# Kernel tuning notes

Hardware: AMD Instinct MI355X
Metric: run time of the kernel (lower is better)

## Reference

```python
import jax, jax.numpy as jnp
import numpy as np

E = 16   # num_experts
K = 4    # num_activated_experts
B, S, H, I = 4, 1024, 1024, 2048


def setup_inputs() -> dict:
    key = jax.random.key(0)
    k0, k1, k2, k3 = jax.random.split(key, 4)
    scale = 0.02
    return {
        "hidden_states": jax.random.normal(k0, (B, S, H), jnp.float32),
        "router_w": jax.random.normal(k1, (H, E), jnp.float32) * scale,
        "router_b": jnp.zeros((E,), jnp.float32),
        "w1": jax.random.normal(k2, (E, H, I), jnp.float32) * scale,
        "b1": jnp.zeros((E, I), jnp.float32),
        "w2": jax.random.normal(k3, (E, I, H), jnp.float32) * scale,
        "b2": jnp.zeros((E, H), jnp.float32),
    }


def reference(hidden_states, router_w, router_b, w1, b1, w2, b2):
    b, s, h = hidden_states.shape
    # router: softmax over experts, pick top-k, renormalize top-k weights
    logits = hidden_states @ router_w + router_b            # [B,S,E]
    probs = jax.nn.softmax(logits, axis=-1)
    topw, topi = jax.lax.top_k(probs, K)                    # [B,S,K]
    topw = topw / jnp.sum(topw, axis=-1, keepdims=True)
    # scatter top-k weights into dense per-expert combine weights [B,S,E]
    combine = jnp.sum(
        jax.nn.one_hot(topi, E, dtype=hidden_states.dtype) * topw[..., None],
        axis=2,
    )
    x = hidden_states.reshape(b * s, h)                     # [T,H]
    c = combine.reshape(b * s, E)                           # [T,E]

    def body(acc, expert):
        w1e, b1e, w2e, b2e, ce = expert
        hmid = jax.nn.gelu(x @ w1e + b1e, approximate=False)  # [T,I]
        return acc + (hmid @ w2e + b2e) * ce[:, None], None

    out, _ = jax.lax.scan(body, jnp.zeros_like(x), (w1, b1, w2, b2, c.T))
    return out.reshape(b, s, h)
```

## Files before the change

kernel.cpp:

```cpp
#include <hip/hip_runtime.h>

#define T_TOK 4096
#define H_DIM 1024
#define I_DIM 2048
#define E_NUM 16
#define K_TOP 4
#define BM 128
#define BK 32
#define MAX_TILES 144
#define PAD_PAIRS (MAX_TILES * BM)
#define RW_Q 4104

typedef __attribute__((ext_vector_type(8))) short s16x8;
typedef __attribute__((ext_vector_type(4))) float f32x4;
typedef __attribute__((ext_vector_type(4))) unsigned short u16x4;
typedef __attribute__((ext_vector_type(8))) unsigned short u16x8;

__device__ __forceinline__ unsigned short f2bf(float f) {
  unsigned u = __float_as_uint(f);
  u += 0x7fffu + ((u >> 16) & 1u);
  return (unsigned short)(u >> 16);
}

__device__ __forceinline__ void mfma_bf16(const s16x8& a, const s16x8& b, f32x4& c) {
  asm("v_mfma_f32_16x16x32_bf16 %0, %1, %2, %0" : "+v"(c) : "v"(a), "v"(b));
}

__device__ __forceinline__ void gld16(const void* g, void* l) {
  __builtin_amdgcn_global_load_lds(
      (const __attribute__((address_space(1))) unsigned int*)g,
      (__attribute__((address_space(3))) unsigned int*)l, 16, 0, 0);
}

__device__ __forceinline__ int tile_map(const int* counts, int ty, int* tsp) {
  int e = -1, acc = 0, base = 0;
#pragma unroll
  for (int ee = 0; ee < E_NUM; ++ee) {
    int tc = (counts[ee] + 127) >> 7;
    if (ty >= acc && ty < acc + tc) {
      e = ee;
      *tsp = base + ((ty - acc) << 7);
    }
    acc += tc;
    base += tc << 7;
  }
  return e;
}

__global__ __launch_bounds__(256) void cvt_kernel(const float* __restrict__ x,
                                                  unsigned short* __restrict__ xb) {
  size_t i = ((size_t)blockIdx.x * 256 + threadIdx.x) * 8;
  f32x4 a = *(const f32x4*)(x + i);
  f32x4 b = *(const f32x4*)(x + i + 4);
  u16x8 o;
  o[0] = f2bf(a[0]); o[1] = f2bf(a[1]); o[2] = f2bf(a[2]); o[3] = f2bf(a[3]);
  o[4] = f2bf(b[0]); o[5] = f2bf(b[1]); o[6] = f2bf(b[2]); o[7] = f2bf(b[3]);
  *(u16x8*)(xb + i) = o;
}

__global__ __launch_bounds__(256) void router_kernel(
    const float* __restrict__ x, const float* __restrict__ rw,
    const float* __restrict__ rb, int* __restrict__ topi,
    float* __restrict__ topw, int* __restrict__ counts) {
  __shared__ float rws[4 * RW_Q];
  const int tid = threadIdx.x;
  for (int idx = tid * 4; idx < H_DIM * E_NUM; idx += 256 * 4) {
    f32x4 v = *(const f32x4*)(rw + idx);
    int h = idx >> 4, e0 = idx & 15;
    *(f32x4*)&rws[(h >> 8) * RW_Q + (h & 255) * 16 + e0] = v;
  }
  __syncthreads();
  const int w = tid >> 6, l = tid & 63;
  const int e = l & 15, q = l >> 4;
  const float rbe = rb[e];
  const float* ldsb = &rws[q * RW_Q + e];
#pragma unroll
  for (int i = 0; i < 4; ++i) {
    const int t = blockIdx.x * 16 + w * 4 + i;
    const float* xr = x + (size_t)t * H_DIM + (q << 8);
    float acc = 0.f;
#pragma unroll 8
    for (int hh = 0; hh < 256; hh += 4) {
      f32x4 xv = *(const f32x4*)(xr + hh);
      acc += xv[0] * ldsb[(hh + 0) * 16];
      acc += xv[1] * ldsb[(hh + 1) * 16];
      acc += xv[2] * ldsb[(hh + 2) * 16];
      acc += xv[3] * ldsb[(hh + 3) * 16];
    }
    acc += __shfl_xor(acc, 16);
    acc += __shfl_xor(acc, 32);
    float logit = acc + rbe;
    float m = logit;
    m = fmaxf(m, __shfl_xor(m, 1));
    m = fmaxf(m, __shfl_xor(m, 2));
    m = fmaxf(m, __shfl_xor(m, 4));
    m = fmaxf(m, __shfl_xor(m, 8));
    float ex = expf(logit - m);
    int rank = 0;
    const int b16 = l & 48;
#pragma unroll
    for (int j = 0; j < 16; ++j) {
      float vj = __shfl(ex, b16 + j);
      rank += (vj > ex) || (vj == ex && j < e);
    }
    float sel = (rank < K_TOP) ? ex : 0.f;
    float subs = sel;
    subs += __shfl_xor(subs, 1);
    subs += __shfl_xor(subs, 2);
    subs += __shfl_xor(subs, 4);
    subs += __shfl_xor(subs, 8);
    if (q == 0 && rank < K_TOP) {
      topi[t * K_TOP + rank] = e;
      topw[t * K_TOP + rank] = ex / subs;
      atomicAdd(&counts[e], 1);
    }
  }
}

__global__ __launch_bounds__(256) void scatter_kernel(
    const int* __restrict__ topi, const float* __restrict__ topw,
    const int* __restrict__ counts, int* __restrict__ cursor,
    int* __restrict__ pairTok, float* __restrict__ pairW,
    int* __restrict__ pairPos) {
  int padBase[E_NUM];
  int base = 0;
#pragma unroll
  for (int ee = 0; ee < E_NUM; ++ee) {
    padBase[ee] = base;
    base += ((counts[ee] + 127) >> 7) << 7;
  }
  int t = blockIdx.x * 256 + threadIdx.x;
  if (t >= T_TOK) return;
#pragma unroll
  for (int k = 0; k < K_TOP; ++k) {
    int e = topi[t * K_TOP + k];
    int pos = atomicAdd(&cursor[e], 1);
    int idx = padBase[e] + pos;
    pairTok[idx] = t;
    pairW[idx] = topw[t * K_TOP + k];
    pairPos[t * K_TOP + k] = idx;
  }
}

__global__ __launch_bounds__(256) void transpose_kernel(
    const float* __restrict__ src, unsigned short* __restrict__ dst, int R,
    int C) {
  size_t es = (size_t)R * C;
  src += es * blockIdx.z;
  dst += es * blockIdx.z;
  int r0 = blockIdx.y * 64, c0 = blockIdx.x * 64;
  __shared__ float tle[64][65];
  int rr = threadIdx.x >> 4, cc = (threadIdx.x & 15) * 4;
#pragma unroll
  for (int i = 0; i < 4; ++i) {
    f32x4 v = *(const f32x4*)(src + (size_t)(r0 + rr + 16 * i) * C + c0 + cc);
    tle[rr + 16 * i][cc + 0] = v[0];
    tle[rr + 16 * i][cc + 1] = v[1];
    tle[rr + 16 * i][cc + 2] = v[2];
    tle[rr + 16 * i][cc + 3] = v[3];
  }
  __syncthreads();
#pragma unroll
  for (int i = 0; i < 4; ++i) {
    int oc = c0 + rr + 16 * i;
    u16x4 o;
    o[0] = f2bf(tle[cc + 0][rr + 16 * i]);
    o[1] = f2bf(tle[cc + 1][rr + 16 * i]);
    o[2] = f2bf(tle[cc + 2][rr + 16 * i]);
    o[3] = f2bf(tle[cc + 3][rr + 16 * i]);
    *(u16x4*)(dst + (size_t)oc * R + r0 + cc) = o;
  }
}

__global__ __launch_bounds__(256, 4) void gemm1_kernel(
    const unsigned short* __restrict__ xb, const unsigned short* __restrict__ w1t,
    const float* __restrict__ b1, unsigned short* __restrict__ hmid,
    const int* __restrict__ pairTok, const int* __restrict__ counts) {
  const int bid = blockIdx.x;
  const int lin = (bid & 7) * 288 + (bid >> 3);
  const int tx = lin & 15, ty = lin >> 4;
  int tsp = 0;
  const int e = tile_map(counts, ty, &tsp);
  if (e < 0) return;
  const int n0 = tx * 128;
  __shared__ unsigned short As[2][BM * BK];
  __shared__ unsigned short Bs[2][BM * BK];
  const int tid = threadIdx.x, w = tid >> 6, l = tid & 63;
  const int rbase = w * 16 + (l >> 2);
  const int segp = (l & 3) ^ ((l >> 3) & 3);
  int tok0 = pairTok[tsp + rbase];
  if (tok0 < 0) tok0 = 0;
  int tok1 = pairTok[tsp + rbase + 64];
  if (tok1 < 0) tok1 = 0;
  const char* gA0 = (const char*)(xb + (size_t)tok0 * H_DIM) + segp * 16;
  const char* gA1 = (const char*)(xb + (size_t)tok1 * H_DIM) + segp * 16;
  const unsigned short* wbase = w1t + (size_t)e * I_DIM * H_DIM;
  const char* gB0 = (const char*)(wbase + (size_t)(n0 + rbase) * H_DIM) + segp * 16;
  const char* gB1 = (const char*)(wbase + (size_t)(n0 + rbase + 64) * H_DIM) + segp * 16;

  f32x4 acc[4][4];
#pragma unroll
  for (int m = 0; m < 4; ++m)
#pragma unroll
    for (int n = 0; n < 4; ++n) acc[m][n] = f32x4{0.f, 0.f, 0.f, 0.f};

  const int wr = w >> 1, wc = w & 1, lrow = l & 15, g = l >> 4;
  const int gs = g ^ ((l >> 1) & 3);
  const int NK = H_DIM / BK;

  gld16(gA0, &As[0][w * 512]);
  gld16(gA1, &As[0][2048 + w * 512]);
  gld16(gB0, &Bs[0][w * 512]);
  gld16(gB1, &Bs[0][2048 + w * 512]);

  for (int kt = 0; kt < NK; ++kt) {
    __syncthreads();
    if (kt + 1 < NK) {
      const int kb = (kt + 1) * 64;
      const int nb = (kt + 1) & 1;
      gld16(gA0 + kb, &As[nb][w * 512]);
      gld16(gA1 + kb, &As[nb][2048 + w * 512]);
      gld16(gB0 + kb, &Bs[nb][w * 512]);
      gld16(gB1 + kb, &Bs[nb][2048 + w * 512]);
    }
    const int cb = kt & 1;
    const s16x8* Ap = (const s16x8*)As[cb];
    const s16x8* Bp = (const s16x8*)Bs[cb];
    s16x8 av[4], bv[4];
#pragma unroll
    for (int m = 0; m < 4; ++m) av[m] = Ap[(wr * 64 + m * 16 + lrow) * 4 + gs];
#pragma unroll
    for (int n = 0; n < 4; ++n) bv[n] = Bp[(wc * 64 + n * 16 + lrow) * 4 + gs];
#pragma unroll
    for (int m = 0; m < 4; ++m)
#pragma unroll
      for (int n = 0; n < 4; ++n) mfma_bf16(av[m], bv[n], acc[m][n]);
  }

  const float* b1e = b1 + (size_t)e * I_DIM;
#pragma unroll
  for (int m = 0; m < 4; ++m) {
    const int rw0 = wr * 64 + m * 16 + g * 4;
#pragma unroll
    for (int n = 0; n < 4; ++n) {
      const int col = n0 + wc * 64 + n * 16 + lrow;
      const float bb = b1e[col];
      f32x4 v = acc[m][n];
#pragma unroll
      for (int j = 0; j < 4; ++j) {
        const int p = tsp + rw0 + j;
        float xv = v[j] + bb;
        float y = 0.7978845608028654f * (xv + 0.044715f * xv * xv * xv);
        float ey = __expf(2.f * y);
        float th = 1.f - 2.f / (ey + 1.f);
        float ge = 0.5f * xv * (1.f + th);
        hmid[(size_t)p * I_DIM + col] = f2bf(ge);
      }
    }
  }
}

__global__ __launch_bounds__(256, 4) void gemm2_kernel(
    const unsigned short* __restrict__ hmid,
    const unsigned short* __restrict__ w2t, const float* __restrict__ b2,
    float* __restrict__ out, unsigned short* __restrict__ poA,
    unsigned short* __restrict__ poB, const int* __restrict__ pairTok,
    const float* __restrict__ pairW, const int* __restrict__ counts, int mode) {
  const int bid = blockIdx.x;
  const int nchunk = (mode == 2) ? 288 : 144;
  const int lin = (bid & 7) * nchunk + (bid >> 3);
  const int kh = (mode == 2) ? (lin & 1) : 0;
  const int tx = (mode == 2) ? ((lin >> 1) & 7) : (lin & 7);
  const int ty = (mode == 2) ? (lin >> 4) : (lin >> 3);
  int tsp = 0;
  const int e = tile_map(counts, ty, &tsp);
  if (e < 0) return;
  const int n0 = tx * 128;
  __shared__ unsigned short As[2][BM * BK];
  __shared__ unsigned short Bs[2][BM * BK];
  const int tid = threadIdx.x, w = tid >> 6, l = tid & 63;
  const int rbase = w * 16 + (l >> 2);
  const int segp = (l & 3) ^ ((l >> 3) & 3);
  const size_t koff = (size_t)kh * 2048;
  const char* gA0 =
      (const char*)(hmid + (size_t)(tsp + rbase) * I_DIM) + segp * 16 + koff;
  const char* gA1 =
      (const char*)(hmid + (size_t)(tsp + rbase + 64) * I_DIM) + segp * 16 + koff;
  const unsigned short* wbase = w2t + (size_t)e * H_DIM * I_DIM;
  const char* gB0 =
      (const char*)(wbase + (size_t)(n0 + rbase) * I_DIM) + segp * 16 + koff;
  const char* gB1 =
      (const char*)(wbase + (size_t)(n0 + rbase + 64) * I_DIM) + segp * 16 + koff;

  f32x4 acc[4][4];
#pragma unroll
  for (int m = 0; m < 4; ++m)
#pragma unroll
    for (int n = 0; n < 4; ++n) acc[m][n] = f32x4{0.f, 0.f, 0.f, 0.f};

  const int wr = w >> 1, wc = w & 1, lrow = l & 15, g = l >> 4;
  const int gs = g ^ ((l >> 1) & 3);
  const int NK = (mode == 2) ? 32 : 64;

  gld16(gA0, &As[0][w * 512]);
  gld16(gA1, &As[0][2048 + w * 512]);
  gld16(gB0, &Bs[0][w * 512]);
  gld16(gB1, &Bs[0][2048 + w * 512]);

  for (int kt = 0; kt < NK; ++kt) {
    __syncthreads();
    if (kt + 1 < NK) {
      const int kb = (kt + 1) * 64;
      const int nb = (kt + 1) & 1;
      gld16(gA0 + kb, &As[nb][w * 512]);
      gld16(gA1 + kb, &As[nb][2048 + w * 512]);
      gld16(gB0 + kb, &Bs[nb][w * 512]);
      gld16(gB1 + kb, &Bs[nb][2048 + w * 512]);
    }
    const int cb = kt & 1;
    const s16x8* Ap = (const s16x8*)As[cb];
    const s16x8* Bp = (const s16x8*)Bs[cb];
    s16x8 av[4], bv[4];
#pragma unroll
    for (int m = 0; m < 4; ++m) av[m] = Ap[(wr * 64 + m * 16 + lrow) * 4 + gs];
#pragma unroll
    for (int n = 0; n < 4; ++n) bv[n] = Bp[(wc * 64 + n * 16 + lrow) * 4 + gs];
#pragma unroll
    for (int m = 0; m < 4; ++m)
#pragma unroll
      for (int n = 0; n < 4; ++n) mfma_bf16(av[m], bv[n], acc[m][n]);
  }

  if (mode >= 1) {
    unsigned short* po = (kh == 0) ? poA : poB;
#pragma unroll
    for (int m = 0; m < 4; ++m) {
      const int rw0 = wr * 64 + m * 16 + g * 4;
#pragma unroll
      for (int n = 0; n < 4; ++n) {
        const int col = n0 + wc * 64 + n * 16 + lrow;
        f32x4 v = acc[m][n];
#pragma unroll
        for (int j = 0; j < 4; ++j)
          po[(size_t)(tsp + rw0 + j) * H_DIM + col] = f2bf(v[j]);
      }
    }
  } else {
    const float* b2e = b2 + (size_t)e * H_DIM;
#pragma unroll
    for (int m = 0; m < 4; ++m) {
      const int rw0 = wr * 64 + m * 16 + g * 4;
#pragma unroll
      for (int j = 0; j < 4; ++j) {
        const int p = tsp + rw0 + j;
        const int tok = pairTok[p];
        if (tok < 0) continue;
        const float pw = pairW[p];
        float* orow = out + (size_t)tok * H_DIM;
#pragma unroll
        for (int n = 0; n < 4; ++n) {
          const int col = n0 + wc * 64 + n * 16 + lrow;
          float val = (acc[m][n][j] + b2e[col]) * pw;
          atomicAdd(orow + col, val);
        }
      }
    }
  }
}

__global__ __launch_bounds__(256) void combine_kernel(
    const unsigned short* __restrict__ poA, const unsigned short* __restrict__ poB,
    const int* __restrict__ pairPos, const int* __restrict__ topi,
    const float* __restrict__ topw, const float* __restrict__ b2,
    float* __restrict__ out, int nbuf) {
  const int t = blockIdx.x * 2 + (threadIdx.x >> 7);
  const int c0 = (threadIdx.x & 127) * 8;
  float o[8];
#pragma unroll
  for (int j = 0; j < 8; ++j) o[j] = 0.f;
#pragma unroll
  for (int k = 0; k < K_TOP; ++k) {
    const int e = topi[t * K_TOP + k];
    const float pw = topw[t * K_TOP + k];
    const int pos = pairPos[t * K_TOP + k];
    u16x8 va = *(const u16x8*)(poA + (size_t)pos * H_DIM + c0);
    u16x8 vb;
    if (nbuf == 2) vb = *(const u16x8*)(poB + (size_t)pos * H_DIM + c0);
    const float* b2r = b2 + (size_t)e * H_DIM + c0;
#pragma unroll
    for (int j = 0; j < 8; ++j) {
      float hv = __uint_as_float((unsigned)va[j] << 16);
      if (nbuf == 2) hv += __uint_as_float((unsigned)vb[j] << 16);
      o[j] += pw * (hv + b2r[j]);
    }
  }
  float* orow = out + (size_t)t * H_DIM + c0;
  *(f32x4*)orow = f32x4{o[0], o[1], o[2], o[3]};
  *(f32x4*)(orow + 4) = f32x4{o[4], o[5], o[6], o[7]};
}

extern "C" void kernel_launch(void* const* d_in, const int* in_sizes, int n_in,
                              void* d_out, int out_size, void* d_ws,
                              size_t ws_size, hipStream_t stream) {
  const float* x = (const float*)d_in[0];
  const float* rw = (const float*)d_in[1];
  const float* rb = (const float*)d_in[2];
  const float* w1 = (const float*)d_in[3];
  const float* b1 = (const float*)d_in[4];
  const float* w2 = (const float*)d_in[5];
  const float* b2 = (const float*)d_in[6];
  float* out = (float*)d_out;
  char* ws = (char*)d_ws;

  const size_t xbSz = (size_t)T_TOK * H_DIM * 2;
  const size_t poSz = (size_t)PAD_PAIRS * H_DIM * 2;
  const size_t wtSz = (size_t)E_NUM * H_DIM * I_DIM * 2;
  const size_t hmSz = (size_t)PAD_PAIRS * I_DIM * 2;
  const size_t smallSz = (size_t)T_TOK * K_TOP * 4 * 3
                         + (size_t)PAD_PAIRS * 4 * 2
                         + 128;
  const size_t needSplit = poSz * 2 + wtSz + hmSz + smallSz;
  const size_t needRich = poSz + wtSz + hmSz + smallSz;
  const size_t needPoor = xbSz + wtSz + hmSz + smallSz;
  int mode = 0;
  if (ws_size >= needSplit) mode = 2;
  else if (ws_size >= needRich) mode = 1;
  else if (ws_size < needPoor) return;

  size_t off = 0;
  unsigned short* xb = (unsigned short*)(ws + off);
  unsigned short* poA = (unsigned short*)(ws + off);
  off += (mode >= 1) ? poSz : xbSz;
  unsigned short* poB = (unsigned short*)(ws + off);
  if (mode == 2) off += poSz;
  unsigned short* wT = (unsigned short*)(ws + off);
  off += wtSz;
  unsigned short* hmid = (unsigned short*)(ws + off);
  off += hmSz;
  int* topi = (int*)(ws + off);      off += (size_t)T_TOK * K_TOP * 4;
  float* topw = (float*)(ws + off);  off += (size_t)T_TOK * K_TOP * 4;
  int* pairPos = (int*)(ws + off);   off += (size_t)T_TOK * K_TOP * 4;
  int* pairTok = (int*)(ws + off);   off += (size_t)PAD_PAIRS * 4;
  float* pairW = (float*)(ws + off); off += (size_t)PAD_PAIRS * 4;
  int* counts = (int*)(ws + off);    off += 64;
  int* cursor = (int*)(ws + off);    off += 64;

  hipMemsetAsync(counts, 0, 128, stream);
  hipMemsetAsync(pairTok, 0xFF, (size_t)PAD_PAIRS * 4, stream);
  if (mode == 0) hipMemsetAsync(out, 0, (size_t)T_TOK * H_DIM * 4, stream);

  cvt_kernel<<<T_TOK * H_DIM / (256 * 8), 256, 0, stream>>>(x, xb);
  router_kernel<<<T_TOK / 16, 256, 0, stream>>>(x, rw, rb, topi, topw, counts);
  scatter_kernel<<<T_TOK / 256, 256, 0, stream>>>(topi, topw, counts, cursor,
                                                  pairTok, pairW, pairPos);
  transpose_kernel<<<dim3(I_DIM / 64, H_DIM / 64, E_NUM), 256, 0, stream>>>(
      w1, wT, H_DIM, I_DIM);
  gemm1_kernel<<<16 * MAX_TILES, 256, 0, stream>>>(xb, wT, b1, hmid, pairTok,
                                                   counts);
  transpose_kernel<<<dim3(H_DIM / 64, I_DIM / 64, E_NUM), 256, 0, stream>>>(
      w2, wT, I_DIM, H_DIM);
  gemm2_kernel<<<(mode == 2 ? 16 : 8) * MAX_TILES, 256, 0, stream>>>(
      hmid, wT, b2, out, poA, poB, pairTok, pairW, counts, mode);
  if (mode >= 1)
    combine_kernel<<<T_TOK / 2, 256, 0, stream>>>(poA, poB, pairPos, topi, topw,
                                                  b2, out, mode);
}
```

Before: 420.2 us.

## Fuse bf16 input conversion into router and merge both weight transposes

Moves the fp32-to-bf16 conversion of the hidden states into the router kernel, which already reads the same rows, and drops the separate conversion launch. When the workspace is large enough, both weight transposes run as a single combined launch into two separate buffers instead of sharing one buffer between the GEMMs. This removes launch overhead and a serialization point between gemm1 and the w2 transpose. The cost is extra workspace for a second transposed weight copy, plus an added conversion loop in each router block.

Result: no change. 417.4 us (-0.7%).

```diff
diff --git a/kernel.cpp b/kernel.cpp
--- a/kernel.cpp
+++ b/kernel.cpp
@@ -47,23 +47,26 @@
   return e;
 }
 
-__global__ __launch_bounds__(256) void cvt_kernel(const float* __restrict__ x,
-                                                  unsigned short* __restrict__ xb) {
-  size_t i = ((size_t)blockIdx.x * 256 + threadIdx.x) * 8;
-  f32x4 a = *(const f32x4*)(x + i);
-  f32x4 b = *(const f32x4*)(x + i + 4);
-  u16x8 o;
-  o[0] = f2bf(a[0]); o[1] = f2bf(a[1]); o[2] = f2bf(a[2]); o[3] = f2bf(a[3]);
-  o[4] = f2bf(b[0]); o[5] = f2bf(b[1]); o[6] = f2bf(b[2]); o[7] = f2bf(b[3]);
-  *(u16x8*)(xb + i) = o;
-}
-
 __global__ __launch_bounds__(256) void router_kernel(
     const float* __restrict__ x, const float* __restrict__ rw,
     const float* __restrict__ rb, int* __restrict__ topi,
-    float* __restrict__ topw, int* __restrict__ counts) {
+    float* __restrict__ topw, int* __restrict__ counts,
+    unsigned short* __restrict__ xb) {
   __shared__ float rws[4 * RW_Q];
   const int tid = threadIdx.x;
+  {
+    const size_t base = (size_t)blockIdx.x * 16 * H_DIM;
+#pragma unroll
+    for (int it = 0; it < 8; ++it) {
+      size_t idx = base + ((size_t)(it * 256 + tid)) * 8;
+      f32x4 a = *(const f32x4*)(x + idx);
+      f32x4 b = *(const f32x4*)(x + idx + 4);
+      u16x8 o;
+      o[0] = f2bf(a[0]); o[1] = f2bf(a[1]); o[2] = f2bf(a[2]); o[3] = f2bf(a[3]);
+      o[4] = f2bf(b[0]); o[5] = f2bf(b[1]); o[6] = f2bf(b[2]); o[7] = f2bf(b[3]);
+      *(u16x8*)(xb + idx) = o;
+    }
+  }
   for (int idx = tid * 4; idx < H_DIM * E_NUM; idx += 256 * 4) {
     f32x4 v = *(const f32x4*)(rw + idx);
     int h = idx >> 4, e0 = idx & 15;
@@ -142,13 +145,10 @@
   }
 }
 
-__global__ __launch_bounds__(256) void transpose_kernel(
-    const float* __restrict__ src, unsigned short* __restrict__ dst, int R,
-    int C) {
-  size_t es = (size_t)R * C;
-  src += es * blockIdx.z;
-  dst += es * blockIdx.z;
-  int r0 = blockIdx.y * 64, c0 = blockIdx.x * 64;
+__device__ __forceinline__ void transpose_tile(const float* __restrict__ src,
+                                               unsigned short* __restrict__ dst,
+                                               int R, int C, int tx, int ty) {
+  int r0 = ty * 64, c0 = tx * 64;
   __shared__ float tle[64][65];
   int rr = threadIdx.x >> 4, cc = (threadIdx.x & 15) * 4;
 #pragma unroll
@@ -169,6 +169,29 @@
     o[2] = f2bf(tle[cc + 2][rr + 16 * i]);
     o[3] = f2bf(tle[cc + 3][rr + 16 * i]);
     *(u16x4*)(dst + (size_t)oc * R + r0 + cc) = o;
+  }
+}
+
+__global__ __launch_bounds__(256) void transpose_kernel(
+    const float* __restrict__ src, unsigned short* __restrict__ dst, int R,
+    int C) {
+  size_t es = (size_t)R * C;
+  transpose_tile(src + es * blockIdx.z, dst + es * blockIdx.z, R, C,
+                 blockIdx.x, blockIdx.y);
+}
+
+__global__ __launch_bounds__(256) void transpose2_kernel(
+    const float* __restrict__ w1, const float* __restrict__ w2,
+    unsigned short* __restrict__ wT1, unsigned short* __restrict__ wT2) {
+  const int bid = blockIdx.x;
+  const size_t es = (size_t)H_DIM * I_DIM;
+  if (bid < 8192) {
+    const int e = bid >> 9, tb = bid & 511;
+    transpose_tile(w1 + es * e, wT1 + es * e, H_DIM, I_DIM, tb & 31, tb >> 5);
+  } else {
+    const int eb = bid - 8192;
+    const int e = eb >> 9, tb = eb & 511;
+    transpose_tile(w2 + es * e, wT2 + es * e, I_DIM, H_DIM, tb & 15, tb >> 4);
   }
 }
 
@@ -419,22 +442,27 @@
   const size_t smallSz = (size_t)T_TOK * K_TOP * 4 * 3
                          + (size_t)PAD_PAIRS * 4 * 2
                          + 128;
-  const size_t needSplit = poSz * 2 + wtSz + hmSz + smallSz;
-  const size_t needRich = poSz + wtSz + hmSz + smallSz;
-  const size_t needPoor = xbSz + wtSz + hmSz + smallSz;
-  int mode = 0;
-  if (ws_size >= needSplit) mode = 2;
-  else if (ws_size >= needRich) mode = 1;
-  else if (ws_size < needPoor) return;
+  const size_t need3 = poSz * 2 + wtSz * 2 + hmSz + smallSz;
+  const size_t need2 = poSz * 2 + wtSz + hmSz + smallSz;
+  const size_t need1 = poSz + wtSz + hmSz + smallSz;
+  const size_t need0 = xbSz + wtSz + hmSz + smallSz;
+  int mode;
+  if (ws_size >= need3) mode = 3;
+  else if (ws_size >= need2) mode = 2;
+  else if (ws_size >= need1) mode = 1;
+  else if (ws_size >= need0) mode = 0;
+  else return;
 
   size_t off = 0;
   unsigned short* xb = (unsigned short*)(ws + off);
   unsigned short* poA = (unsigned short*)(ws + off);
   off += (mode >= 1) ? poSz : xbSz;
   unsigned short* poB = (unsigned short*)(ws + off);
-  if (mode == 2) off += poSz;
-  unsigned short* wT = (unsigned short*)(ws + off);
+  if (mode >= 2) off += poSz;
+  unsigned short* wT1 = (unsigned short*)(ws + off);
   off += wtSz;
+  unsigned short* wT2 = wT1;
+  if (mode == 3) { wT2 = (unsigned short*)(ws + off); off += wtSz; }
   unsigned short* hmid = (unsigned short*)(ws + off);
   off += hmSz;
   int* topi = (int*)(ws + off);      off += (size_t)T_TOK * K_TOP * 4;
@@ -445,23 +473,31 @@
   int* counts = (int*)(ws + off);    off += 64;
   int* cursor = (int*)(ws + off);    off += 64;
 
+  const int gmode = (mode >= 2) ? 2 : mode;
+
   hipMemsetAsync(counts, 0, 128, stream);
   hipMemsetAsync(pairTok, 0xFF, (size_t)PAD_PAIRS * 4, stream);
-  if (mode == 0) hipMemsetAsync(out, 0, (size_t)T_TOK * H_DIM * 4, stream);
-
-  cvt_kernel<<<T_TOK * H_DIM / (256 * 8), 256, 0, stream>>>(x, xb);
-  router_kernel<<<T_TOK / 16, 256, 0, stream>>>(x, rw, rb, topi, topw, counts);
+  if (gmode == 0) hipMemsetAsync(out, 0, (size_t)T_TOK * H_DIM * 4, stream);
+
+  router_kernel<<<T_TOK / 16, 256, 0, stream>>>(x, rw, rb, topi, topw, counts,
+                                                xb);
   scatter_kernel<<<T_TOK / 256, 256, 0, stream>>>(topi, topw, counts, cursor,
                                                   pairTok, pairW, pairPos);
-  transpose_kernel<<<dim3(I_DIM / 64, H_DIM / 64, E_NUM), 256, 0, stream>>>(
-      w1, wT, H_DIM, I_DIM);
-  gemm1_kernel<<<16 * MAX_TILES, 256, 0, stream>>>(xb, wT, b1, hmid, pairTok,
-                                                   counts);
-  transpose_kernel<<<dim3(H_DIM / 64, I_DIM / 64, E_NUM), 256, 0, stream>>>(
-      w2, wT, I_DIM, H_DIM);
-  gemm2_kernel<<<(mode == 2 ? 16 : 8) * MAX_TILES, 256, 0, stream>>>(
-      hmid, wT, b2, out, poA, poB, pairTok, pairW, counts, mode);
-  if (mode >= 1)
+  if (mode == 3) {
+    transpose2_kernel<<<16384, 256, 0, stream>>>(w1, w2, wT1, wT2);
+    gemm1_kernel<<<16 * MAX_TILES, 256, 0, stream>>>(xb, wT1, b1, hmid, pairTok,
+                                                     counts);
+  } else {
+    transpose_kernel<<<dim3(I_DIM / 64, H_DIM / 64, E_NUM), 256, 0, stream>>>(
+        w1, wT1, H_DIM, I_DIM);
+    gemm1_kernel<<<16 * MAX_TILES, 256, 0, stream>>>(xb, wT1, b1, hmid, pairTok,
+                                                     counts);
+    transpose_kernel<<<dim3(H_DIM / 64, I_DIM / 64, E_NUM), 256, 0, stream>>>(
+        w2, wT2, I_DIM, H_DIM);
+  }
+  gemm2_kernel<<<(gmode == 2 ? 16 : 8) * MAX_TILES, 256, 0, stream>>>(
+      hmid, wT2, b2, out, poA, poB, pairTok, pairW, counts, gmode);
+  if (gmode >= 1)
     combine_kernel<<<T_TOK / 2, 256, 0, stream>>>(poA, poB, pairPos, topi, topw,
-                                                  b2, out, mode);
-}
+                                                  b2, out, gmode);
+}
```
